# Kernel tuning notes

Hardware: AMD Instinct MI355X
Metric: run time of the kernel (lower is better)

## Reference

```python
import jax, jax.numpy as jnp
import numpy as np

EMBED_DIM = 512
NUM_HEADS = 8
HEAD_DIM = EMBED_DIM // NUM_HEADS


def setup_inputs() -> dict:
    key = jax.random.key(0)
    k1, k2, kw, kb, kow, kob = jax.random.split(key, 6)
    B, L, C = 2, 2048, EMBED_DIM
    s = 1.0 / np.sqrt(C)
    return {
        "x1": jax.random.normal(k1, (B, L, C), dtype=jnp.float32),
        "x2": jax.random.normal(k2, (B, L, C), dtype=jnp.float32),
        # nn.Linear(embed_dim, 3*embed_dim): weight [3C, C], bias [3C]
        "qkv_w": jax.random.uniform(kw, (3 * C, C), jnp.float32, -s, s),
        "qkv_b": jax.random.uniform(kb, (3 * C,), jnp.float32, -s, s),
        # nn.Linear(embed_dim, embed_dim): weight [C, C], bias [C]
        "out_w": jax.random.uniform(kow, (C, C), jnp.float32, -s, s),
        "out_b": jax.random.uniform(kob, (C,), jnp.float32, -s, s),
    }


def _qkv(x, qkv_w, qkv_b):
    B, L, C = x.shape
    H, D = NUM_HEADS, C // NUM_HEADS
    # Linear: x @ W^T + b, then view(B, L, H, 3, D) and split along the '3' axis
    qkv = (jnp.einsum("blc,fc->blf", x, qkv_w) + qkv_b).reshape(B, L, H, 3, D)
    qkv = jnp.transpose(qkv, (3, 0, 2, 1, 4))  # [3, B, H, L, D]
    return qkv[0], qkv[1], qkv[2]


def _attend(q, k, v):
    # q,k,v: [B, H, L, D]; scale by 1/sqrt(D)
    scale = 1.0 / np.sqrt(q.shape[-1]).astype(np.float32)
    scores = jnp.einsum("bhqd,bhkd->bhqk", q, k) * scale  # [B,H,L,L]
    attn = jax.nn.softmax(scores, axis=-1)
    out = jnp.einsum("bhqk,bhkd->bhqd", attn, v)
    B, H, L, D = out.shape
    return jnp.transpose(out, (0, 2, 1, 3)).reshape(B, L, H * D)


def reference(x1, x2, qkv_w, qkv_b, out_w, out_b):
    q1, k1, v1 = _qkv(x1, qkv_w, qkv_b)
    q2, k2, v2 = _qkv(x2, qkv_w, qkv_b)
    out1 = _attend(q1, k2, v2)  # q from x1, k/v from x2
    out2 = _attend(q2, k1, v1)  # q from x2, k/v from x1
    out1 = jnp.einsum("blc,fc->blf", out1, out_w) + out_b
    out2 = jnp.einsum("blc,fc->blf", out2, out_w) + out_b
    return (out1, out2)
```

## Files before the change

### kernel.cpp

```cpp
#include <hip/hip_runtime.h>
#include <stdint.h>

typedef unsigned short u16;
typedef unsigned int u32;
typedef short bf16x8 __attribute__((ext_vector_type(8)));
typedef float f32x4 __attribute__((ext_vector_type(4)));
typedef float f32x16 __attribute__((ext_vector_type(16)));

#define K_DIM 512

__device__ __forceinline__ u16 f2bf(float f) {
  union { float f; u32 u; } v; v.f = f;
  return (u16)((v.u + 0x8000u) >> 16);
}
__device__ __forceinline__ u32 pk2(float lo, float hi) {
  union { float f; u32 u; } a, b; a.f = lo; b.f = hi;
  return __builtin_amdgcn_perm(b.u + 0x8000u, a.u + 0x8000u, 0x07060302u);
}

__global__ void cvt_kernel(const float* __restrict__ x1, const float* __restrict__ x2,
                           const float* __restrict__ qkvw, const float* __restrict__ outw,
                           u16* __restrict__ xb, u16* __restrict__ wqkv, u16* __restrict__ wout) {
  int tid = blockIdx.x * 256 + threadIdx.x;
  const float4* src; u16* dst; int idx = tid;
  if (idx < 524288)        { src = (const float4*)x1;   dst = xb; }
  else if (idx < 1048576)  { src = (const float4*)x2;   dst = xb + 2097152; idx -= 524288; }
  else if (idx < 1245184)  { src = (const float4*)qkvw; dst = wqkv;         idx -= 1048576; }
  else                     { src = (const float4*)outw; dst = wout;         idx -= 1245184; }
  float4 v = src[idx];
  *(uint2*)&dst[idx * 4] = make_uint2(pk2(v.x, v.y), pk2(v.z, v.w));
}

#define LDA 40

__global__ __launch_bounds__(256, 3) void qkv_gemm(
    const u16* __restrict__ A, const u16* __restrict__ W, const float* __restrict__ bias,
    u16* __restrict__ qb, u16* __restrict__ kb, u16* __restrict__ vtb) {
  __shared__ __align__(16) u16 As[2][128 * LDA];
  __shared__ __align__(16) u16 Bs[2][128 * LDA];
  const int t = threadIdx.x;
  const int m0 = blockIdx.x * 128, n0 = blockIdx.y * 128;
  const int lane = t & 63, l16 = lane & 15, quad = lane >> 4;
  const int w = t >> 6;
  const int wm = (w >> 1) * 64, wn = (w & 1) * 64;
  const int sr = t >> 2, sc = (t & 3) * 8;

  const u16* Ap = A + (size_t)(m0 + sr) * K_DIM + sc;
  const u16* Wp = W + (size_t)(n0 + sr) * K_DIM + sc;

  f32x4 acc[4][4];
#pragma unroll
  for (int i = 0; i < 4; ++i)
#pragma unroll
    for (int j = 0; j < 4; ++j) acc[i][j] = (f32x4){0.f, 0.f, 0.f, 0.f};

  uint4 ra0 = *(const uint4*)(Ap);
  uint4 ra1 = *(const uint4*)(Ap + 64 * K_DIM);
  uint4 rb0 = *(const uint4*)(Wp);
  uint4 rb1 = *(const uint4*)(Wp + 64 * K_DIM);
  *(uint4*)&As[0][sr * LDA + sc] = ra0;
  *(uint4*)&As[0][(sr + 64) * LDA + sc] = ra1;
  *(uint4*)&Bs[0][sr * LDA + sc] = rb0;
  *(uint4*)&Bs[0][(sr + 64) * LDA + sc] = rb1;
  ra0 = *(const uint4*)(Ap + 32);
  ra1 = *(const uint4*)(Ap + 64 * K_DIM + 32);
  rb0 = *(const uint4*)(Wp + 32);
  rb1 = *(const uint4*)(Wp + 64 * K_DIM + 32);
  __syncthreads();

  for (int kt = 0; kt < 16; ++kt) {
    const int cur = kt & 1, nxt = cur ^ 1;
    if (kt < 15) {
      *(uint4*)&As[nxt][sr * LDA + sc] = ra0;
      *(uint4*)&As[nxt][(sr + 64) * LDA + sc] = ra1;
      *(uint4*)&Bs[nxt][sr * LDA + sc] = rb0;
      *(uint4*)&Bs[nxt][(sr + 64) * LDA + sc] = rb1;
    }
    if (kt < 14) {
      int ko = (kt + 2) * 32;
      ra0 = *(const uint4*)(Ap + ko);
      ra1 = *(const uint4*)(Ap + 64 * K_DIM + ko);
      rb0 = *(const uint4*)(Wp + ko);
      rb1 = *(const uint4*)(Wp + 64 * K_DIM + ko);
    }
    bf16x8 af[4], bfr[4];
#pragma unroll
    for (int mi = 0; mi < 4; ++mi)
      af[mi] = *(const bf16x8*)&As[cur][(wm + mi * 16 + l16) * LDA + quad * 8];
#pragma unroll
    for (int ni = 0; ni < 4; ++ni)
      bfr[ni] = *(const bf16x8*)&Bs[cur][(wn + ni * 16 + l16) * LDA + quad * 8];
#pragma unroll
    for (int mi = 0; mi < 4; ++mi)
#pragma unroll
      for (int ni = 0; ni < 4; ++ni)
        acc[mi][ni] = __builtin_amdgcn_mfma_f32_16x16x32_bf16(bfr[ni], af[mi], acc[mi][ni], 0, 0, 0);
    __syncthreads();
  }

  const int fbase = n0 + wn;
  const int h = fbase / 192;
  const int s = (fbase - h * 192) >> 6;
  float4 bv[4];
#pragma unroll
  for (int ni = 0; ni < 4; ++ni)
    bv[ni] = *(const float4*)&bias[fbase + ni * 16 + quad * 4];
  const int bh = m0 >> 11;
  const int lbase = (m0 & 2047) + wm;

  if (s == 2) {
    u16* dst = vtb + (size_t)((bh * 8 + h) * 64) * 2048;
#pragma unroll
    for (int mi = 0; mi < 4; ++mi) {
      int l = lbase + mi * 16 + l16;
#pragma unroll
      for (int ni = 0; ni < 4; ++ni)
#pragma unroll
        for (int r = 0; r < 4; ++r)
          dst[(ni * 16 + quad * 4 + r) * 2048 + l] = f2bf(acc[mi][ni][r] + bv[ni][r]);
    }
  } else {
    u16* dst = (s == 0 ? qb : kb) + (size_t)((bh * 8 + h) * 2048) * 64;
    const float sc2 = (s == 0) ? 0.18033688011112042f : 1.0f;
#pragma unroll
    for (int mi = 0; mi < 4; ++mi) {
      int l = lbase + mi * 16 + l16;
#pragma unroll
      for (int ni = 0; ni < 4; ++ni) {
        float v0 = (acc[mi][ni][0] + bv[ni][0]) * sc2;
        float v1 = (acc[mi][ni][1] + bv[ni][1]) * sc2;
        float v2 = (acc[mi][ni][2] + bv[ni][2]) * sc2;
        float v3 = (acc[mi][ni][3] + bv[ni][3]) * sc2;
        *(uint2*)&dst[(size_t)l * 64 + ni * 16 + quad * 4] = make_uint2(pk2(v0, v1), pk2(v2, v3));
      }
    }
  }
}

#define LQ 72
#define LP 72

__global__ __launch_bounds__(256, 2) void attn_kernel(
    const u16* __restrict__ qb, const u16* __restrict__ kb, const u16* __restrict__ vtb,
    u16* __restrict__ attnb) {
  __shared__ __align__(16) u16 Ks[64 * LQ];
  __shared__ __align__(16) u16 VTs[64 * LQ];
  __shared__ __align__(16) u16 Ps[128 * LP];

  const int t = threadIdx.x;
  const int w = t >> 6, lane = t & 63, l32 = lane & 31, h2 = lane >> 5;
  const int bid = blockIdx.x;
  const int comb = bid & 31;
  const int qt = bid >> 5;
  const int h = comb & 7, bb = (comb >> 3) & 1, pair = comb >> 4;
  const int in_q = pair, in_kv = pair ^ 1;

  const u16* Qg = qb + (size_t)((in_q * 2 + bb) * 8 + h) * 2048 * 64;
  const u16* Kg = kb + (size_t)((in_kv * 2 + bb) * 8 + h) * 2048 * 64;
  const u16* Vg = vtb + (size_t)((in_kv * 2 + bb) * 8 + h) * 64 * 2048;

#pragma unroll
  for (int u = 0; u < 4; ++u) {
    int idx = u * 256 + t;
    int row = idx >> 3, seg = (idx & 7) * 8;
    *(uint4*)&Ps[row * LP + seg] = *(const uint4*)(Qg + (qt * 128 + row) * 64 + seg);
  }
  const int srow = t >> 3, sseg = (t & 7) * 8;
  uint4 rk0 = *(const uint4*)(Kg + srow * 64 + sseg);
  uint4 rk1 = *(const uint4*)(Kg + (srow + 32) * 64 + sseg);
  uint4 rv0 = *(const uint4*)(Vg + srow * 2048 + sseg);
  uint4 rv1 = *(const uint4*)(Vg + (srow + 32) * 2048 + sseg);
  __syncthreads();

  bf16x8 qf[4];
#pragma unroll
  for (int ks = 0; ks < 4; ++ks)
    qf[ks] = *(const bf16x8*)&Ps[(w * 32 + l32) * LP + ks * 16 + h2 * 8];

  f32x16 oacc[2];
#pragma unroll
  for (int mi = 0; mi < 2; ++mi)
#pragma unroll
    for (int r = 0; r < 16; ++r) oacc[mi][r] = 0.f;
  float rs = 0.f;

  u16* Pw = &Ps[w * 32 * LP];

  for (int kt = 0; kt < 32; ++kt) {
    *(uint4*)&Ks[srow * LQ + sseg] = rk0;
    *(uint4*)&Ks[(srow + 32) * LQ + sseg] = rk1;
    *(uint4*)&VTs[srow * LQ + sseg] = rv0;
    *(uint4*)&VTs[(srow + 32) * LQ + sseg] = rv1;
    __syncthreads();
    if (kt < 31) {
      int ko = (kt + 1) * 64;
      rk0 = *(const uint4*)(Kg + (ko + srow) * 64 + sseg);
      rk1 = *(const uint4*)(Kg + (ko + srow + 32) * 64 + sseg);
      rv0 = *(const uint4*)(Vg + srow * 2048 + ko + sseg);
      rv1 = *(const uint4*)(Vg + (srow + 32) * 2048 + ko + sseg);
    }

    f32x16 sacc[2];
#pragma unroll
    for (int mi = 0; mi < 2; ++mi)
#pragma unroll
      for (int r = 0; r < 16; ++r) sacc[mi][r] = 0.f;
#pragma unroll
    for (int ks = 0; ks < 4; ++ks) {
      bf16x8 kfr0 = *(const bf16x8*)&Ks[(l32) * LQ + ks * 16 + h2 * 8];
      bf16x8 kfr1 = *(const bf16x8*)&Ks[(32 + l32) * LQ + ks * 16 + h2 * 8];
      sacc[0] = __builtin_amdgcn_mfma_f32_32x32x16_bf16(kfr0, qf[ks], sacc[0], 0, 0, 0);
      sacc[1] = __builtin_amdgcn_mfma_f32_32x32x16_bf16(kfr1, qf[ks], sacc[1], 0, 0, 0);
    }

#pragma unroll
    for (int mi = 0; mi < 2; ++mi)
#pragma unroll
      for (int rg = 0; rg < 4; ++rg) {
        float p0 = __builtin_amdgcn_exp2f(sacc[mi][rg * 4 + 0]);
        float p1 = __builtin_amdgcn_exp2f(sacc[mi][rg * 4 + 1]);
        float p2 = __builtin_amdgcn_exp2f(sacc[mi][rg * 4 + 2]);
        float p3 = __builtin_amdgcn_exp2f(sacc[mi][rg * 4 + 3]);
        rs += (p0 + p1) + (p2 + p3);
        *(uint2*)&Pw[l32 * LP + mi * 32 + rg * 8 + h2 * 4] = make_uint2(pk2(p0, p1), pk2(p2, p3));
      }

#pragma unroll
    for (int ks = 0; ks < 4; ++ks) {
      bf16x8 pf = *(const bf16x8*)&Pw[l32 * LP + ks * 16 + h2 * 8];
      bf16x8 vf0 = *(const bf16x8*)&VTs[(l32) * LQ + ks * 16 + h2 * 8];
      bf16x8 vf1 = *(const bf16x8*)&VTs[(32 + l32) * LQ + ks * 16 + h2 * 8];
      oacc[0] = __builtin_amdgcn_mfma_f32_32x32x16_bf16(vf0, pf, oacc[0], 0, 0, 0);
      oacc[1] = __builtin_amdgcn_mfma_f32_32x32x16_bf16(vf1, pf, oacc[1], 0, 0, 0);
    }
    __syncthreads();
  }

  rs += __shfl_xor(rs, 32);
  const float inv = 1.0f / rs;
  const int row = in_q * 4096 + bb * 2048 + qt * 128 + w * 32 + l32;
#pragma unroll
  for (int mi = 0; mi < 2; ++mi)
#pragma unroll
    for (int rg = 0; rg < 4; ++rg) {
      float v0 = oacc[mi][rg * 4 + 0] * inv;
      float v1 = oacc[mi][rg * 4 + 1] * inv;
      float v2 = oacc[mi][rg * 4 + 2] * inv;
      float v3 = oacc[mi][rg * 4 + 3] * inv;
      *(uint2*)&attnb[(size_t)row * 512 + h * 64 + mi * 32 + rg * 8 + h2 * 4] =
          make_uint2(pk2(v0, v1), pk2(v2, v3));
    }
}

__global__ __launch_bounds__(256, 2) void out_gemm(
    const u16* __restrict__ A, const u16* __restrict__ W, const float* __restrict__ bias,
    float* __restrict__ out) {
  __shared__ __align__(16) u16 As[2][64 * LDA];
  __shared__ __align__(16) u16 Bs[2][128 * LDA];
  const int t = threadIdx.x;
  const int m0 = blockIdx.x * 64, n0 = blockIdx.y * 128;
  const int lane = t & 63, l16 = lane & 15, quad = lane >> 4;
  const int w = t >> 6;
  const int wm = (w & 1) * 32, wn = (w >> 1) * 64;
  const int ar = t >> 2, ac = (t & 3) * 8;
  const int sr = t >> 2, sc = (t & 3) * 8;

  const u16* Ap = A + (size_t)(m0 + ar) * K_DIM + ac;
  const u16* Wp = W + (size_t)(n0 + sr) * K_DIM + sc;

  f32x4 acc[2][4];
#pragma unroll
  for (int i = 0; i < 2; ++i)
#pragma unroll
    for (int j = 0; j < 4; ++j) acc[i][j] = (f32x4){0.f, 0.f, 0.f, 0.f};

  uint4 ra = *(const uint4*)Ap;
  uint4 rb0 = *(const uint4*)(Wp);
  uint4 rb1 = *(const uint4*)(Wp + 64 * K_DIM);
  *(uint4*)&As[0][ar * LDA + ac] = ra;
  *(uint4*)&Bs[0][sr * LDA + sc] = rb0;
  *(uint4*)&Bs[0][(sr + 64) * LDA + sc] = rb1;
  ra = *(const uint4*)(Ap + 32);
  rb0 = *(const uint4*)(Wp + 32);
  rb1 = *(const uint4*)(Wp + 64 * K_DIM + 32);
  __syncthreads();

  for (int kt = 0; kt < 16; ++kt) {
    const int cur = kt & 1, nxt = cur ^ 1;
    if (kt < 15) {
      *(uint4*)&As[nxt][ar * LDA + ac] = ra;
      *(uint4*)&Bs[nxt][sr * LDA + sc] = rb0;
      *(uint4*)&Bs[nxt][(sr + 64) * LDA + sc] = rb1;
    }
    if (kt < 14) {
      int ko = (kt + 2) * 32;
      ra = *(const uint4*)(Ap + ko);
      rb0 = *(const uint4*)(Wp + ko);
      rb1 = *(const uint4*)(Wp + 64 * K_DIM + ko);
    }
    bf16x8 af[2], bfr[4];
#pragma unroll
    for (int mi = 0; mi < 2; ++mi)
      af[mi] = *(const bf16x8*)&As[cur][(wm + mi * 16 + l16) * LDA + quad * 8];
#pragma unroll
    for (int ni = 0; ni < 4; ++ni)
      bfr[ni] = *(const bf16x8*)&Bs[cur][(wn + ni * 16 + l16) * LDA + quad * 8];
#pragma unroll
    for (int mi = 0; mi < 2; ++mi)
#pragma unroll
      for (int ni = 0; ni < 4; ++ni)
        acc[mi][ni] = __builtin_amdgcn_mfma_f32_16x16x32_bf16(af[mi], bfr[ni], acc[mi][ni], 0, 0, 0);
    __syncthreads();
  }

#pragma unroll
  for (int ni = 0; ni < 4; ++ni) {
    int f = n0 + wn + ni * 16 + l16;
    float bv = bias[f];
#pragma unroll
    for (int mi = 0; mi < 2; ++mi)
#pragma unroll
      for (int r = 0; r < 4; ++r) {
        int m = m0 + wm + mi * 16 + quad * 4 + r;
        out[(size_t)m * 512 + f] = acc[mi][ni][r] + bv;
      }
  }
}

extern "C" void kernel_launch(void* const* d_in, const int* in_sizes, int n_in,
                              void* d_out, int out_size, void* d_ws, size_t ws_size,
                              hipStream_t stream) {
  const float* x1   = (const float*)d_in[0];
  const float* x2   = (const float*)d_in[1];
  const float* qkvw = (const float*)d_in[2];
  const float* qkvb = (const float*)d_in[3];
  const float* outw = (const float*)d_in[4];
  const float* outb = (const float*)d_in[5];
  float* out = (float*)d_out;
  char* ws = (char*)d_ws;

  u16* xb    = (u16*)(ws + 0);
  u16* wqkv  = (u16*)(ws + 8388608);
  u16* wout  = (u16*)(ws + 9961472);
  u16* qb    = (u16*)(ws + 10485760);
  u16* kb    = (u16*)(ws + 18874368);
  u16* vtb   = (u16*)(ws + 27262976);
  u16* attnb = (u16*)(ws + 0);

  cvt_kernel<<<5120, 256, 0, stream>>>(x1, x2, qkvw, outw, xb, wqkv, wout);

  dim3 g1(64, 12);
  qkv_gemm<<<g1, 256, 0, stream>>>(xb, wqkv, qkvb, qb, kb, vtb);

  attn_kernel<<<512, 256, 0, stream>>>(qb, kb, vtb, attnb);

  dim3 g3(128, 4);
  out_gemm<<<g3, 256, 0, stream>>>(attnb, wout, outb, out);
}
```

Before: 156.3 us.

## Load GEMM tiles straight into LDS via global_load_lds, single-buffered, higher occupancy

Both GEMM kernels now copy global tiles directly into shared memory with global_load_lds. This replaces the register-staged double-buffered prefetch with one unpadded single buffer and a barrier per k-step. Launch bounds rise to 4 blocks per CU, so occupancy rather than the software pipeline has to hide memory latency. The bf16 packing helper also switches to the HIP __float22bfloat162_rn conversion. The risks are LDS bank conflicts from dropping the padding and load latency that is no longer overlapped within a block.

After: 158.6 us. Within noise of the previous version (+1.5%).

```diff
diff --git a/kernel.cpp b/kernel.cpp
--- a/kernel.cpp
+++ b/kernel.cpp
@@ -1,4 +1,5 @@
 #include <hip/hip_runtime.h>
+#include <hip/hip_bf16.h>
 #include <stdint.h>
 
 typedef unsigned short u16;
@@ -13,9 +14,14 @@
   union { float f; u32 u; } v; v.f = f;
   return (u16)((v.u + 0x8000u) >> 16);
 }
-__device__ __forceinline__ u32 pk2(float lo, float hi) {
-  union { float f; u32 u; } a, b; a.f = lo; b.f = hi;
-  return __builtin_amdgcn_perm(b.u + 0x8000u, a.u + 0x8000u, 0x07060302u);
+__device__ __forceinline__ u32 pkcvt(float lo, float hi) {
+  union { __hip_bfloat162 h; u32 u; } c;
+  c.h = __float22bfloat162_rn(float2{lo, hi});
+  return c.u;
+}
+__device__ __forceinline__ void gl_lds16(const u16* g, u16* l) {
+  __builtin_amdgcn_global_load_lds((const __attribute__((address_space(1))) void*)g,
+                                   (__attribute__((address_space(3))) void*)l, 16, 0, 0);
 }
 
 __global__ void cvt_kernel(const float* __restrict__ x1, const float* __restrict__ x2,
@@ -28,16 +34,16 @@
   else if (idx < 1245184)  { src = (const float4*)qkvw; dst = wqkv;         idx -= 1048576; }
   else                     { src = (const float4*)outw; dst = wout;         idx -= 1245184; }
   float4 v = src[idx];
-  *(uint2*)&dst[idx * 4] = make_uint2(pk2(v.x, v.y), pk2(v.z, v.w));
-}
-
-#define LDA 40
-
-__global__ __launch_bounds__(256, 3) void qkv_gemm(
+  *(uint2*)&dst[idx * 4] = make_uint2(pkcvt(v.x, v.y), pkcvt(v.z, v.w));
+}
+
+#define LDA 32
+
+__global__ __launch_bounds__(256, 4) void qkv_gemm(
     const u16* __restrict__ A, const u16* __restrict__ W, const float* __restrict__ bias,
     u16* __restrict__ qb, u16* __restrict__ kb, u16* __restrict__ vtb) {
-  __shared__ __align__(16) u16 As[2][128 * LDA];
-  __shared__ __align__(16) u16 Bs[2][128 * LDA];
+  __shared__ __align__(16) u16 As[128 * LDA];
+  __shared__ __align__(16) u16 Bs[128 * LDA];
   const int t = threadIdx.x;
   const int m0 = blockIdx.x * 128, n0 = blockIdx.y * 128;
   const int lane = t & 63, l16 = lane & 15, quad = lane >> 4;
@@ -47,6 +53,8 @@
 
   const u16* Ap = A + (size_t)(m0 + sr) * K_DIM + sc;
   const u16* Wp = W + (size_t)(n0 + sr) * K_DIM + sc;
+  u16* AsT = &As[t * 8];
+  u16* BsT = &Bs[t * 8];
 
   f32x4 acc[4][4];
 #pragma unroll
@@ -54,42 +62,20 @@
 #pragma unroll
     for (int j = 0; j < 4; ++j) acc[i][j] = (f32x4){0.f, 0.f, 0.f, 0.f};
 
-  uint4 ra0 = *(const uint4*)(Ap);
-  uint4 ra1 = *(const uint4*)(Ap + 64 * K_DIM);
-  uint4 rb0 = *(const uint4*)(Wp);
-  uint4 rb1 = *(const uint4*)(Wp + 64 * K_DIM);
-  *(uint4*)&As[0][sr * LDA + sc] = ra0;
-  *(uint4*)&As[0][(sr + 64) * LDA + sc] = ra1;
-  *(uint4*)&Bs[0][sr * LDA + sc] = rb0;
-  *(uint4*)&Bs[0][(sr + 64) * LDA + sc] = rb1;
-  ra0 = *(const uint4*)(Ap + 32);
-  ra1 = *(const uint4*)(Ap + 64 * K_DIM + 32);
-  rb0 = *(const uint4*)(Wp + 32);
-  rb1 = *(const uint4*)(Wp + 64 * K_DIM + 32);
-  __syncthreads();
-
   for (int kt = 0; kt < 16; ++kt) {
-    const int cur = kt & 1, nxt = cur ^ 1;
-    if (kt < 15) {
-      *(uint4*)&As[nxt][sr * LDA + sc] = ra0;
-      *(uint4*)&As[nxt][(sr + 64) * LDA + sc] = ra1;
-      *(uint4*)&Bs[nxt][sr * LDA + sc] = rb0;
-      *(uint4*)&Bs[nxt][(sr + 64) * LDA + sc] = rb1;
-    }
-    if (kt < 14) {
-      int ko = (kt + 2) * 32;
-      ra0 = *(const uint4*)(Ap + ko);
-      ra1 = *(const uint4*)(Ap + 64 * K_DIM + ko);
-      rb0 = *(const uint4*)(Wp + ko);
-      rb1 = *(const uint4*)(Wp + 64 * K_DIM + ko);
-    }
+    const int ko = kt * 32;
+    gl_lds16(Ap + ko, AsT);
+    gl_lds16(Ap + 64 * K_DIM + ko, AsT + 64 * LDA);
+    gl_lds16(Wp + ko, BsT);
+    gl_lds16(Wp + 64 * K_DIM + ko, BsT + 64 * LDA);
+    __syncthreads();
     bf16x8 af[4], bfr[4];
 #pragma unroll
     for (int mi = 0; mi < 4; ++mi)
-      af[mi] = *(const bf16x8*)&As[cur][(wm + mi * 16 + l16) * LDA + quad * 8];
+      af[mi] = *(const bf16x8*)&As[(wm + mi * 16 + l16) * LDA + quad * 8];
 #pragma unroll
     for (int ni = 0; ni < 4; ++ni)
-      bfr[ni] = *(const bf16x8*)&Bs[cur][(wn + ni * 16 + l16) * LDA + quad * 8];
+      bfr[ni] = *(const bf16x8*)&Bs[(wn + ni * 16 + l16) * LDA + quad * 8];
 #pragma unroll
     for (int mi = 0; mi < 4; ++mi)
 #pragma unroll
@@ -131,7 +117,7 @@
         float v1 = (acc[mi][ni][1] + bv[ni][1]) * sc2;
         float v2 = (acc[mi][ni][2] + bv[ni][2]) * sc2;
         float v3 = (acc[mi][ni][3] + bv[ni][3]) * sc2;
-        *(uint2*)&dst[(size_t)l * 64 + ni * 16 + quad * 4] = make_uint2(pk2(v0, v1), pk2(v2, v3));
+        *(uint2*)&dst[(size_t)l * 64 + ni * 16 + quad * 4] = make_uint2(pkcvt(v0, v1), pkcvt(v2, v3));
       }
     }
   }
@@ -222,7 +208,7 @@
         float p2 = __builtin_amdgcn_exp2f(sacc[mi][rg * 4 + 2]);
         float p3 = __builtin_amdgcn_exp2f(sacc[mi][rg * 4 + 3]);
         rs += (p0 + p1) + (p2 + p3);
-        *(uint2*)&Pw[l32 * LP + mi * 32 + rg * 8 + h2 * 4] = make_uint2(pk2(p0, p1), pk2(p2, p3));
+        *(uint2*)&Pw[l32 * LP + mi * 32 + rg * 8 + h2 * 4] = make_uint2(pkcvt(p0, p1), pkcvt(p2, p3));
       }
 
 #pragma unroll
@@ -248,25 +234,26 @@
       float v2 = oacc[mi][rg * 4 + 2] * inv;
       float v3 = oacc[mi][rg * 4 + 3] * inv;
       *(uint2*)&attnb[(size_t)row * 512 + h * 64 + mi * 32 + rg * 8 + h2 * 4] =
-          make_uint2(pk2(v0, v1), pk2(v2, v3));
-    }
-}
-
-__global__ __launch_bounds__(256, 2) void out_gemm(
+          make_uint2(pkcvt(v0, v1), pkcvt(v2, v3));
+    }
+}
+
+__global__ __launch_bounds__(256, 4) void out_gemm(
     const u16* __restrict__ A, const u16* __restrict__ W, const float* __restrict__ bias,
     float* __restrict__ out) {
-  __shared__ __align__(16) u16 As[2][64 * LDA];
-  __shared__ __align__(16) u16 Bs[2][128 * LDA];
+  __shared__ __align__(16) u16 As[64 * LDA];
+  __shared__ __align__(16) u16 Bs[128 * LDA];
   const int t = threadIdx.x;
   const int m0 = blockIdx.x * 64, n0 = blockIdx.y * 128;
   const int lane = t & 63, l16 = lane & 15, quad = lane >> 4;
   const int w = t >> 6;
   const int wm = (w & 1) * 32, wn = (w >> 1) * 64;
-  const int ar = t >> 2, ac = (t & 3) * 8;
   const int sr = t >> 2, sc = (t & 3) * 8;
 
-  const u16* Ap = A + (size_t)(m0 + ar) * K_DIM + ac;
+  const u16* Ap = A + (size_t)(m0 + sr) * K_DIM + sc;
   const u16* Wp = W + (size_t)(n0 + sr) * K_DIM + sc;
+  u16* AsT = &As[t * 8];
+  u16* BsT = &Bs[t * 8];
 
   f32x4 acc[2][4];
 #pragma unroll
@@ -274,37 +261,19 @@
 #pragma unroll
     for (int j = 0; j < 4; ++j) acc[i][j] = (f32x4){0.f, 0.f, 0.f, 0.f};
 
-  uint4 ra = *(const uint4*)Ap;
-  uint4 rb0 = *(const uint4*)(Wp);
-  uint4 rb1 = *(const uint4*)(Wp + 64 * K_DIM);
-  *(uint4*)&As[0][ar * LDA + ac] = ra;
-  *(uint4*)&Bs[0][sr * LDA + sc] = rb0;
-  *(uint4*)&Bs[0][(sr + 64) * LDA + sc] = rb1;
-  ra = *(const uint4*)(Ap + 32);
-  rb0 = *(const uint4*)(Wp + 32);
-  rb1 = *(const uint4*)(Wp + 64 * K_DIM + 32);
-  __syncthreads();
-
   for (int kt = 0; kt < 16; ++kt) {
-    const int cur = kt & 1, nxt = cur ^ 1;
-    if (kt < 15) {
-      *(uint4*)&As[nxt][ar * LDA + ac] = ra;
-      *(uint4*)&Bs[nxt][sr * LDA + sc] = rb0;
-      *(uint4*)&Bs[nxt][(sr + 64) * LDA + sc] = rb1;
-    }
-    if (kt < 14) {
-      int ko = (kt + 2) * 32;
-      ra = *(const uint4*)(Ap + ko);
-      rb0 = *(const uint4*)(Wp + ko);
-      rb1 = *(const uint4*)(Wp + 64 * K_DIM + ko);
-    }
+    const int ko = kt * 32;
+    gl_lds16(Ap + ko, AsT);
+    gl_lds16(Wp + ko, BsT);
+    gl_lds16(Wp + 64 * K_DIM + ko, BsT + 64 * LDA);
+    __syncthreads();
     bf16x8 af[2], bfr[4];
 #pragma unroll
     for (int mi = 0; mi < 2; ++mi)
-      af[mi] = *(const bf16x8*)&As[cur][(wm + mi * 16 + l16) * LDA + quad * 8];
+      af[mi] = *(const bf16x8*)&As[(wm + mi * 16 + l16) * LDA + quad * 8];
 #pragma unroll
     for (int ni = 0; ni < 4; ++ni)
-      bfr[ni] = *(const bf16x8*)&Bs[cur][(wn + ni * 16 + l16) * LDA + quad * 8];
+      bfr[ni] = *(const bf16x8*)&Bs[(wn + ni * 16 + l16) * LDA + quad * 8];
 #pragma unroll
     for (int mi = 0; mi < 2; ++mi)
 #pragma unroll
```
